# Kernel optimization log

Measured on AMD Instinct MI355X. Metric: run time of the kernel, lower is better.

Reference implementation:

```python
import jax, jax.numpy as jnp
import numpy as np

D = 1024
H = 16
HD = D // H
T = 2048  # tgt_len
S = 2048  # src_len
B = 2


def setup_inputs() -> dict:
    key = jax.random.key(0)
    ks = jax.random.split(key, 8)
    w_scale = (6.0 / (D + D)) ** 0.5  # xavier_uniform bound scale (use normal*small for simplicity)
    inp = {
        "query": jax.random.normal(ks[0], (T, B, D), jnp.float32),
        "key": jax.random.normal(ks[1], (S, B, D), jnp.float32),
        "value": jax.random.normal(ks[2], (S, B, D), jnp.float32),
        "Wq": jax.random.normal(ks[3], (D, D), jnp.float32) * w_scale,
        "bq": jnp.zeros((D,), jnp.float32),
        "Wk": jax.random.normal(ks[4], (D, D), jnp.float32) * w_scale,
        "bk": jnp.zeros((D,), jnp.float32),
        "Wv": jax.random.normal(ks[5], (D, D), jnp.float32) * w_scale,
        "bv": jnp.zeros((D,), jnp.float32),
        "Wo": jax.random.normal(ks[6], (D, D), jnp.float32) * w_scale,
        "bo": jnp.zeros((D,), jnp.float32),
    }
    return inp


def reference(query, key, value, Wq, bq, Wk, bk, Wv, bv, Wo, bo):
    tgt_len, bsz, d = query.shape
    src_len = key.shape[0]
    num_heads, head_dim = H, HD
    scaling = head_dim ** -0.5

    # torch Linear: x @ W.T + b
    q = query @ Wq.T + bq   # [T, B, D]
    k = key @ Wk.T + bk     # [S, B, D]
    v = value @ Wv.T + bv   # [S, B, D]

    q = (q * scaling).reshape(tgt_len, bsz, num_heads, head_dim)
    k = k.reshape(src_len, bsz, num_heads, head_dim)
    v = v.reshape(src_len, bsz, num_heads, head_dim)

    # scores: [B, H, T, S]
    scores = jnp.einsum("tbhd,sbhd->bhts", q, k)
    attn = jax.nn.softmax(scores, axis=-1)
    # dropout_p = 0.0 -> no-op

    # attention output: [T, B, H, HD] -> [T, B, D]
    out = jnp.einsum("bhts,sbhd->tbhd", attn, v).reshape(tgt_len, bsz, d)
    Z = out @ Wo.T + bo  # [T, B, D]

    attn_avg = attn.sum(axis=1) / num_heads  # [B, T, S]
    return Z, attn_avg
```

## Files before the change

### kernel.cpp

```cpp
#include <hip/hip_runtime.h>
#include <hip/hip_bf16.h>
#include <math.h>

#define DD    1024
#define NHEAD 16
#define HDIM  64
#define TLEN  2048
#define SLEN  2048
#define BSZ   2
#define NBH   (BSZ*NHEAD)
#define GROWS (TLEN*BSZ)

typedef _Float16 half8 __attribute__((ext_vector_type(8)));
typedef _Float16 half4v __attribute__((ext_vector_type(4)));
typedef float f32x4 __attribute__((ext_vector_type(4)));

#define MFMA16(a,b,c) __builtin_amdgcn_mfma_f32_16x16x32_f16((a),(b),(c),0,0,0)

#define GLD16(g, l) __builtin_amdgcn_global_load_lds( \
    (const __attribute__((address_space(1))) unsigned int*)(g), \
    (__attribute__((address_space(3))) unsigned int*)(l), 16, 0, 0)

__device__ __forceinline__ int swz(int row, int col2) { return col2 ^ ((row & 7) << 4); }

__global__ __launch_bounds__(256) void convk(const float* __restrict__ s,
                                             _Float16* __restrict__ d, int n8) {
    int i = blockIdx.x * 256 + threadIdx.x;
    if (i >= n8) return;
    const float4* s4 = (const float4*)s;
    float4 a = s4[2*i], b = s4[2*i+1];
    half8 v;
    v[0]=(_Float16)a.x; v[1]=(_Float16)a.y; v[2]=(_Float16)a.z; v[3]=(_Float16)a.w;
    v[4]=(_Float16)b.x; v[5]=(_Float16)b.y; v[6]=(_Float16)b.z; v[7]=(_Float16)b.w;
    *(half8*)&d[8*i] = v;
}

__global__ __launch_bounds__(256) void gemm16(const _Float16* __restrict__ A,
        const _Float16* __restrict__ Bw, const float* __restrict__ bias,
        void* __restrict__ Yp, float scale, int f32out) {
    __shared__ _Float16 As[128*32];
    __shared__ _Float16 Bs[128*32];
    const int tid = threadIdx.x;
    const int lane = tid & 63, w = tid >> 6;
    const int l15 = lane & 15, g = lane >> 4;
    const int m0 = blockIdx.y * 128, n0 = blockIdx.x * 128;
    const int wm = (w >> 1) * 64, wn = (w & 1) * 64;

    f32x4 acc[4][4];
    #pragma unroll
    for (int i = 0; i < 4; ++i)
        #pragma unroll
        for (int j = 0; j < 4; ++j) acc[i][j] = (f32x4){0.f,0.f,0.f,0.f};

    for (int kt = 0; kt < DD/32; ++kt) {
        #pragma unroll
        for (int it = 0; it < 2; ++it) {
            int X = (it*256 + tid) * 16;
            int row = X >> 6, xin = X & 63;
            GLD16(A  + (size_t)(m0+row)*DD + kt*32 + (xin>>1), (char*)As + X);
            GLD16(Bw + (size_t)(n0+row)*DD + kt*32 + (xin>>1), (char*)Bs + X);
        }
        __syncthreads();
        half8 af[4], bf[4];
        #pragma unroll
        for (int i = 0; i < 4; ++i)
            af[i] = *(const half8*)((const char*)As + (wm+16*i+l15)*64 + 16*g);
        #pragma unroll
        for (int j = 0; j < 4; ++j)
            bf[j] = *(const half8*)((const char*)Bs + (wn+16*j+l15)*64 + 16*g);
        #pragma unroll
        for (int i = 0; i < 4; ++i)
            #pragma unroll
            for (int j = 0; j < 4; ++j)
                acc[i][j] = MFMA16(af[i], bf[j], acc[i][j]);
        __syncthreads();
    }

    #pragma unroll
    for (int j = 0; j < 4; ++j) {
        int c = n0 + wn + 16*j + l15;
        float bj = bias[c];
        #pragma unroll
        for (int i = 0; i < 4; ++i) {
            #pragma unroll
            for (int r = 0; r < 4; ++r) {
                int rr = m0 + wm + 16*i + 4*g + r;
                float y = (acc[i][j][r] + bj) * scale;
                if (f32out) ((float*)Yp)[(size_t)rr*DD + c] = y;
                else        ((_Float16*)Yp)[(size_t)rr*DD + c] = (_Float16)y;
            }
        }
    }
}

__global__ __launch_bounds__(256) void transv(const _Float16* __restrict__ Vp,
                                              _Float16* __restrict__ Vt) {
    __shared__ _Float16 Ts[64*64];
    const int tid = threadIdx.x;
    const int s0 = blockIdx.x * 64, bh = blockIdx.y;
    const int b = bh >> 4, h = bh & 15;
    #pragma unroll
    for (int it = 0; it < 2; ++it) {
        int X = (it*256 + tid) * 16;
        int row = X >> 7, xin = X & 127;
        int col2 = swz(row, xin);
        GLD16(Vp + (size_t)((s0+row)*2 + b)*DD + h*64 + (col2>>1), (char*)Ts + X);
    }
    __syncthreads();
    const int d = tid >> 2, sp = tid & 3;
    unsigned int wb[8];
    #pragma unroll
    for (int k = 0; k < 16; ++k) {
        int s = sp*16 + k;
        unsigned short u = *(const unsigned short*)((const char*)Ts + s*128 + swz(s, d*2));
        if (k & 1) wb[k>>1] |= ((unsigned int)u) << 16;
        else       wb[k>>1] = u;
    }
    unsigned int* op = (unsigned int*)(Vt + ((size_t)bh*64 + d)*SLEN + s0 + sp*16);
    ((uint4*)op)[0] = make_uint4(wb[0],wb[1],wb[2],wb[3]);
    ((uint4*)op)[1] = make_uint4(wb[4],wb[5],wb[6],wb[7]);
}

__global__ __launch_bounds__(256) void att_o(const _Float16* __restrict__ Qp,
        const _Float16* __restrict__ Kp, const _Float16* __restrict__ Vt,
        _Float16* __restrict__ Op, float* __restrict__ Ml, float* __restrict__ Il) {
    __shared__ char smem[32768];
    _Float16* Ks  = (_Float16*)smem;
    _Float16* Vts = (_Float16*)(smem + 8192);
    const int tid = threadIdx.x;
    const int lane = tid & 63, w = tid >> 6;
    const int l15 = lane & 15, g = lane >> 4;
    const int bh = blockIdx.y, b = bh >> 4, h = bh & 15;
    const int t0 = blockIdx.x * 128;

    half8 qf[2][2];
    #pragma unroll
    for (int nf = 0; nf < 2; ++nf) {
        int t = t0 + w*32 + 16*nf + l15;
        #pragma unroll
        for (int kq = 0; kq < 2; ++kq)
            qf[nf][kq] = *(const half8*)(Qp + (size_t)(t*2+b)*DD + h*64 + 8*g + 32*kq);
    }

    float m[2] = {-1e30f, -1e30f}, l[2] = {0.f, 0.f};
    f32x4 O[4][2];
    #pragma unroll
    for (int dm = 0; dm < 4; ++dm)
        #pragma unroll
        for (int nf = 0; nf < 2; ++nf) O[dm][nf] = (f32x4){0.f,0.f,0.f,0.f};

    for (int s0 = 0; s0 < SLEN; s0 += 64) {
        #pragma unroll
        for (int it = 0; it < 2; ++it) {
            int X = (it*256 + tid) * 16;
            int row = X >> 7, xin = X & 127;
            int col2 = swz(row, xin);
            GLD16(Kp + (size_t)((s0+row)*2 + b)*DD + h*64 + (col2>>1), (char*)Ks + X);
            GLD16(Vt + ((size_t)bh*64 + row)*SLEN + s0 + (col2>>1), (char*)Vts + X);
        }
        __syncthreads();

        f32x4 sc[4][2];
        #pragma unroll
        for (int mf = 0; mf < 4; ++mf) {
            int srow = 16*mf + l15, sw = (srow & 7) << 4;
            half8 k0 = *(const half8*)((const char*)Ks + srow*128 + ((16*g) ^ sw));
            half8 k1 = *(const half8*)((const char*)Ks + srow*128 + ((64 + 16*g) ^ sw));
            #pragma unroll
            for (int nf = 0; nf < 2; ++nf) {
                f32x4 z = (f32x4){0.f,0.f,0.f,0.f};
                z = MFMA16(k0, qf[nf][0], z);
                z = MFMA16(k1, qf[nf][1], z);
                sc[mf][nf] = z;
            }
        }

        half8 pbf[2][2];
        #pragma unroll
        for (int nf = 0; nf < 2; ++nf) {
            float mx = -1e30f;
            #pragma unroll
            for (int mf = 0; mf < 4; ++mf)
                #pragma unroll
                for (int r = 0; r < 4; ++r) mx = fmaxf(mx, sc[mf][nf][r]);
            mx = fmaxf(mx, __shfl_xor(mx, 16));
            mx = fmaxf(mx, __shfl_xor(mx, 32));
            float mn = fmaxf(m[nf], mx);
            float corr = __expf(m[nf] - mn);
            float pr[4][4];
            float rs = 0.f;
            #pragma unroll
            for (int mf = 0; mf < 4; ++mf)
                #pragma unroll
                for (int r = 0; r < 4; ++r) {
                    pr[mf][r] = __expf(sc[mf][nf][r] - mn);
                    rs += pr[mf][r];
                }
            rs += __shfl_xor(rs, 16);
            rs += __shfl_xor(rs, 32);
            l[nf] = l[nf] * corr + rs;
            m[nf] = mn;
            #pragma unroll
            for (int dm = 0; dm < 4; ++dm) O[dm][nf] *= corr;
            #pragma unroll
            for (int kv = 0; kv < 2; ++kv) {
                half8 pb;
                #pragma unroll
                for (int e = 0; e < 4; ++e) {
                    pb[e]   = (_Float16)pr[2*kv][e];
                    pb[4+e] = (_Float16)pr[2*kv+1][e];
                }
                pbf[nf][kv] = pb;
            }
        }

        #pragma unroll
        for (int dm = 0; dm < 4; ++dm) {
            int dl = 16*dm + l15, sw = (dl & 7) << 4;
            #pragma unroll
            for (int kv = 0; kv < 2; ++kv) {
                half4v a0 = *(const half4v*)((const char*)Vts + dl*128 + ((64*kv + 8*g) ^ sw));
                half4v a1 = *(const half4v*)((const char*)Vts + dl*128 + ((64*kv + 32 + 8*g) ^ sw));
                half8 va;
                #pragma unroll
                for (int e = 0; e < 4; ++e) { va[e] = a0[e]; va[4+e] = a1[e]; }
                #pragma unroll
                for (int nf = 0; nf < 2; ++nf)
                    O[dm][nf] = MFMA16(va, pbf[nf][kv], O[dm][nf]);
            }
        }
        __syncthreads();
    }

    float inv[2];
    #pragma unroll
    for (int nf = 0; nf < 2; ++nf) {
        inv[nf] = 1.f / l[nf];
        #pragma unroll
        for (int dm = 0; dm < 4; ++dm) O[dm][nf] *= inv[nf];
    }
    if (g == 0) {
        #pragma unroll
        for (int nf = 0; nf < 2; ++nf) {
            int t = t0 + w*32 + 16*nf + l15;
            Ml[(size_t)bh*TLEN + t] = m[nf];
            Il[(size_t)bh*TLEN + t] = inv[nf];
        }
    }

    float* ow = (float*)smem;
    #pragma unroll
    for (int nf = 0; nf < 2; ++nf) {
        int tl = w*32 + 16*nf + l15;
        #pragma unroll
        for (int dm = 0; dm < 4; ++dm)
            *(f32x4*)&ow[tl*64 + 16*dm + 4*g] = O[dm][nf];
    }
    __syncthreads();
    {
        int trow = tid >> 1, half = tid & 1;
        const float4* rp = (const float4*)(ow + trow*64 + half*32);
        _Float16* gp = Op + (size_t)((t0+trow)*2 + b)*DD + h*64 + half*32;
        #pragma unroll
        for (int c = 0; c < 4; ++c) {
            float4 x = rp[2*c], y = rp[2*c+1];
            half8 o;
            o[0]=(_Float16)x.x; o[1]=(_Float16)x.y; o[2]=(_Float16)x.z; o[3]=(_Float16)x.w;
            o[4]=(_Float16)y.x; o[5]=(_Float16)y.y; o[6]=(_Float16)y.z; o[7]=(_Float16)y.w;
            ((half8*)gp)[c] = o;
        }
    }
}

__global__ __launch_bounds__(256) void att_avg(const _Float16* __restrict__ Qp,
        const _Float16* __restrict__ Kp, const float* __restrict__ Ml,
        const float* __restrict__ Il, float* __restrict__ avg) {
    __shared__ char smem[32768];
    _Float16* Ks = (_Float16*)smem;
    const int tid = threadIdx.x;
    const int lane = tid & 63, w = tid >> 6;
    const int l15 = lane & 15, g = lane >> 4;
    const int b = blockIdx.z;
    const int t0 = blockIdx.y * 128, s0 = blockIdx.x * 128;

    float acc[8][2][4];
    #pragma unroll
    for (int mf = 0; mf < 8; ++mf)
        #pragma unroll
        for (int nf = 0; nf < 2; ++nf)
            #pragma unroll
            for (int r = 0; r < 4; ++r) acc[mf][nf][r] = 0.f;

    for (int h = 0; h < NHEAD; ++h) {
        const int bh = b*NHEAD + h;
        #pragma unroll
        for (int it = 0; it < 4; ++it) {
            int X = (it*256 + tid) * 16;
            int row = X >> 7, xin = X & 127;
            int col2 = swz(row, xin);
            GLD16(Kp + (size_t)((s0+row)*2 + b)*DD + h*64 + (col2>>1), (char*)Ks + X);
        }
        __syncthreads();

        half8 qf[2][2];
        float mm[2], ii[2];
        #pragma unroll
        for (int nf = 0; nf < 2; ++nf) {
            int t = t0 + w*32 + 16*nf + l15;
            #pragma unroll
            for (int kq = 0; kq < 2; ++kq)
                qf[nf][kq] = *(const half8*)(Qp + (size_t)(t*2+b)*DD + h*64 + 8*g + 32*kq);
            mm[nf] = Ml[(size_t)bh*TLEN + t];
            ii[nf] = Il[(size_t)bh*TLEN + t];
        }

        #pragma unroll
        for (int mf = 0; mf < 8; ++mf) {
            int srow = 16*mf + l15, sw = (srow & 7) << 4;
            half8 k0 = *(const half8*)((const char*)Ks + srow*128 + ((16*g) ^ sw));
            half8 k1 = *(const half8*)((const char*)Ks + srow*128 + ((64 + 16*g) ^ sw));
            #pragma unroll
            for (int nf = 0; nf < 2; ++nf) {
                f32x4 z = (f32x4){0.f,0.f,0.f,0.f};
                z = MFMA16(k0, qf[nf][0], z);
                z = MFMA16(k1, qf[nf][1], z);
                #pragma unroll
                for (int r = 0; r < 4; ++r)
                    acc[mf][nf][r] += __expf(z[r] - mm[nf]) * ii[nf];
            }
        }
        __syncthreads();
    }

    const float invh = 1.f / NHEAD;
    float* ow = (float*)smem;
    #pragma unroll
    for (int P = 0; P < 2; ++P) {
        __syncthreads();
        #pragma unroll
        for (int nf = 0; nf < 2; ++nf) {
            int tl = 16*nf + l15;
            #pragma unroll
            for (int mf2 = 0; mf2 < 4; ++mf2) {
                int mf = 4*P + mf2;
                f32x4 v;
                #pragma unroll
                for (int r = 0; r < 4; ++r) v[r] = acc[mf][nf][r] * invh;
                *(f32x4*)&ow[w*2048 + tl*64 + 16*mf2 + 4*g] = v;
            }
        }
        __syncthreads();
        int trow = tid >> 1, half = tid & 1;
        const float4* rp = (const float4*)(ow + (trow>>5)*2048 + (trow&31)*64 + half*32);
        float4* gp = (float4*)(avg + ((size_t)(b*TLEN + t0 + trow))*SLEN + s0 + P*64 + half*32);
        #pragma unroll
        for (int c = 0; c < 8; ++c) gp[c] = rp[c];
    }
}

extern "C" void kernel_launch(void* const* d_in, const int* in_sizes, int n_in,
                              void* d_out, int out_size, void* d_ws, size_t ws_size,
                              hipStream_t stream) {
    (void)in_sizes; (void)n_in; (void)out_size; (void)ws_size;
    const float* query = (const float*)d_in[0];
    const float* key_  = (const float*)d_in[1];
    const float* value = (const float*)d_in[2];
    const float* Wq = (const float*)d_in[3];  const float* bq = (const float*)d_in[4];
    const float* Wk = (const float*)d_in[5];  const float* bk = (const float*)d_in[6];
    const float* Wv = (const float*)d_in[7];  const float* bv = (const float*)d_in[8];
    const float* Wo = (const float*)d_in[9];  const float* bo = (const float*)d_in[10];

    float* out = (float*)d_out;
    char* ws = (char*)d_ws;
    _Float16* QF  = (_Float16*)(ws);
    _Float16* KF  = (_Float16*)(ws + 8388608);
    _Float16* VF  = (_Float16*)(ws + 16777216);
    _Float16* WqF = (_Float16*)(ws + 25165824);
    _Float16* WkF = (_Float16*)(ws + 27262976);
    _Float16* WvF = (_Float16*)(ws + 29360128);
    _Float16* WoF = (_Float16*)(ws + 31457280);
    _Float16* Qp  = (_Float16*)(ws + 33554432);
    _Float16* Kp  = (_Float16*)(ws + 41943040);
    _Float16* Vp  = (_Float16*)(ws + 50331648);
    _Float16* Vt  = (_Float16*)(ws + 58720256);
    float*    Ml  = (float*)(ws + 67108864);
    float*    Il  = (float*)(ws + 67371008);
    _Float16* Op  = QF;

    const dim3 blk(256);
    convk<<<2048, blk, 0, stream>>>(query, QF, 524288);
    convk<<<2048, blk, 0, stream>>>(key_,  KF, 524288);
    convk<<<2048, blk, 0, stream>>>(value, VF, 524288);
    convk<<<512,  blk, 0, stream>>>(Wq, WqF, 131072);
    convk<<<512,  blk, 0, stream>>>(Wk, WkF, 131072);
    convk<<<512,  blk, 0, stream>>>(Wv, WvF, 131072);
    convk<<<512,  blk, 0, stream>>>(Wo, WoF, 131072);

    const dim3 ggrid(8, 32);
    gemm16<<<ggrid, blk, 0, stream>>>(QF, WqF, bq, Qp, 0.125f, 0);
    gemm16<<<ggrid, blk, 0, stream>>>(KF, WkF, bk, Kp, 1.0f,   0);
    gemm16<<<ggrid, blk, 0, stream>>>(VF, WvF, bv, Vp, 1.0f,   0);

    transv<<<dim3(32, 32), blk, 0, stream>>>(Vp, Vt);
    att_o<<<dim3(16, 32), blk, 0, stream>>>(Qp, Kp, Vt, Op, Ml, Il);
    att_avg<<<dim3(16, 16, 2), blk, 0, stream>>>(Qp, Kp, Ml, Il, out + 4194304);

    gemm16<<<ggrid, blk, 0, stream>>>(Op, WoF, bo, out, 1.0f, 1);
}
```

Baseline: 361.7 us.

## Batch conversions and QKV GEMMs, halve attention tiles, deepen GEMM K-step

```diff
diff --git a/kernel.cpp b/kernel.cpp
--- a/kernel.cpp
+++ b/kernel.cpp
@@ -12,7 +12,6 @@
 #define GROWS (TLEN*BSZ)
 
 typedef _Float16 half8 __attribute__((ext_vector_type(8)));
-typedef _Float16 half4v __attribute__((ext_vector_type(4)));
 typedef float f32x4 __attribute__((ext_vector_type(4)));
 
 #define MFMA16(a,b,c) __builtin_amdgcn_mfma_f32_16x16x32_f16((a),(b),(c),0,0,0)
@@ -23,27 +22,28 @@
 
 __device__ __forceinline__ int swz(int row, int col2) { return col2 ^ ((row & 7) << 4); }
 
-__global__ __launch_bounds__(256) void convk(const float* __restrict__ s,
-                                             _Float16* __restrict__ d, int n8) {
-    int i = blockIdx.x * 256 + threadIdx.x;
-    if (i >= n8) return;
-    const float4* s4 = (const float4*)s;
-    float4 a = s4[2*i], b = s4[2*i+1];
+struct CvtArgs { const float* s[7]; _Float16* d[7]; };
+
+__global__ __launch_bounds__(256) void convall(CvtArgs a) {
+    int idx = blockIdx.x * 256 + threadIdx.x;
+    int ai, wi;
+    if (idx < 1572864) { ai = idx / 524288; wi = idx - ai * 524288; }
+    else { int r = idx - 1572864; ai = 3 + (r >> 17); wi = r & 131071; }
+    const float4* s4 = (const float4*)a.s[ai];
+    float4 x = s4[2*wi], y = s4[2*wi+1];
     half8 v;
-    v[0]=(_Float16)a.x; v[1]=(_Float16)a.y; v[2]=(_Float16)a.z; v[3]=(_Float16)a.w;
-    v[4]=(_Float16)b.x; v[5]=(_Float16)b.y; v[6]=(_Float16)b.z; v[7]=(_Float16)b.w;
-    *(half8*)&d[8*i] = v;
-}
-
-__global__ __launch_bounds__(256) void gemm16(const _Float16* __restrict__ A,
-        const _Float16* __restrict__ Bw, const float* __restrict__ bias,
-        void* __restrict__ Yp, float scale, int f32out) {
-    __shared__ _Float16 As[128*32];
-    __shared__ _Float16 Bs[128*32];
+    v[0]=(_Float16)x.x; v[1]=(_Float16)x.y; v[2]=(_Float16)x.z; v[3]=(_Float16)x.w;
+    v[4]=(_Float16)y.x; v[5]=(_Float16)y.y; v[6]=(_Float16)y.z; v[7]=(_Float16)y.w;
+    *(half8*)&a.d[ai][8*wi] = v;
+}
+
+__device__ __forceinline__ void gemm_body(_Float16* As, _Float16* Bs,
+        const _Float16* __restrict__ A, const _Float16* __restrict__ Bw,
+        const float* __restrict__ bias, void* __restrict__ Yp,
+        float scale, int f32out, int m0, int n0) {
     const int tid = threadIdx.x;
     const int lane = tid & 63, w = tid >> 6;
     const int l15 = lane & 15, g = lane >> 4;
-    const int m0 = blockIdx.y * 128, n0 = blockIdx.x * 128;
     const int wm = (w >> 1) * 64, wn = (w & 1) * 64;
 
     f32x4 acc[4][4];
@@ -52,27 +52,30 @@
         #pragma unroll
         for (int j = 0; j < 4; ++j) acc[i][j] = (f32x4){0.f,0.f,0.f,0.f};
 
-    for (int kt = 0; kt < DD/32; ++kt) {
-        #pragma unroll
-        for (int it = 0; it < 2; ++it) {
+    for (int kt = 0; kt < DD/64; ++kt) {
+        #pragma unroll
+        for (int it = 0; it < 4; ++it) {
             int X = (it*256 + tid) * 16;
-            int row = X >> 6, xin = X & 63;
-            GLD16(A  + (size_t)(m0+row)*DD + kt*32 + (xin>>1), (char*)As + X);
-            GLD16(Bw + (size_t)(n0+row)*DD + kt*32 + (xin>>1), (char*)Bs + X);
-        }
-        __syncthreads();
-        half8 af[4], bf[4];
-        #pragma unroll
-        for (int i = 0; i < 4; ++i)
-            af[i] = *(const half8*)((const char*)As + (wm+16*i+l15)*64 + 16*g);
-        #pragma unroll
-        for (int j = 0; j < 4; ++j)
-            bf[j] = *(const half8*)((const char*)Bs + (wn+16*j+l15)*64 + 16*g);
-        #pragma unroll
-        for (int i = 0; i < 4; ++i)
+            int row = X >> 7, xin = X & 127;
+            GLD16(A  + (size_t)(m0+row)*DD + kt*64 + (xin>>1), (char*)As + X);
+            GLD16(Bw + (size_t)(n0+row)*DD + kt*64 + (xin>>1), (char*)Bs + X);
+        }
+        __syncthreads();
+        #pragma unroll
+        for (int kq = 0; kq < 2; ++kq) {
+            half8 af[4], bf[4];
+            #pragma unroll
+            for (int i = 0; i < 4; ++i)
+                af[i] = *(const half8*)((const char*)As + (wm+16*i+l15)*128 + 16*g + 64*kq);
             #pragma unroll
             for (int j = 0; j < 4; ++j)
-                acc[i][j] = MFMA16(af[i], bf[j], acc[i][j]);
+                bf[j] = *(const half8*)((const char*)Bs + (wn+16*j+l15)*128 + 16*g + 64*kq);
+            #pragma unroll
+            for (int i = 0; i < 4; ++i)
+                #pragma unroll
+                for (int j = 0; j < 4; ++j)
+                    acc[i][j] = MFMA16(af[i], bf[j], acc[i][j]);
+        }
         __syncthreads();
     }
 
@@ -93,6 +96,30 @@
     }
 }
 
+__global__ __launch_bounds__(256) void gemm_qkv(
+        const _Float16* QF, const _Float16* KF, const _Float16* VF,
+        const _Float16* WqF, const _Float16* WkF, const _Float16* WvF,
+        const float* bq, const float* bk, const float* bv,
+        _Float16* Qp, _Float16* Kp, _Float16* Vp) {
+    __shared__ _Float16 As[128*64];
+    __shared__ _Float16 Bs[128*64];
+    const int z = blockIdx.z;
+    const _Float16* A  = (z == 0) ? QF  : (z == 1) ? KF  : VF;
+    const _Float16* Wm = (z == 0) ? WqF : (z == 1) ? WkF : WvF;
+    const float*    bi = (z == 0) ? bq  : (z == 1) ? bk  : bv;
+    _Float16*       Y  = (z == 0) ? Qp  : (z == 1) ? Kp  : Vp;
+    float scale = (z == 0) ? 0.125f : 1.0f;
+    gemm_body(As, Bs, A, Wm, bi, Y, scale, 0, blockIdx.y*128, blockIdx.x*128);
+}
+
+__global__ __launch_bounds__(256) void gemm_out(const _Float16* __restrict__ A,
+        const _Float16* __restrict__ Wm, const float* __restrict__ bi,
+        float* __restrict__ Y) {
+    __shared__ _Float16 As[128*64];
+    __shared__ _Float16 Bs[128*64];
+    gemm_body(As, Bs, A, Wm, bi, Y, 1.0f, 1, blockIdx.y*128, blockIdx.x*128);
+}
+
 __global__ __launch_bounds__(256) void transv(const _Float16* __restrict__ Vp,
                                               _Float16* __restrict__ Vt) {
     __shared__ _Float16 Ts[64*64];
@@ -108,46 +135,43 @@
     }
     __syncthreads();
     const int d = tid >> 2, sp = tid & 3;
-    unsigned int wb[8];
-    #pragma unroll
-    for (int k = 0; k < 16; ++k) {
-        int s = sp*16 + k;
-        unsigned short u = *(const unsigned short*)((const char*)Ts + s*128 + swz(s, d*2));
-        if (k & 1) wb[k>>1] |= ((unsigned int)u) << 16;
-        else       wb[k>>1] = u;
-    }
-    unsigned int* op = (unsigned int*)(Vt + ((size_t)bh*64 + d)*SLEN + s0 + sp*16);
-    ((uint4*)op)[0] = make_uint4(wb[0],wb[1],wb[2],wb[3]);
-    ((uint4*)op)[1] = make_uint4(wb[4],wb[5],wb[6],wb[7]);
+    _Float16* rowp = Vt + ((size_t)bh*64 + d)*SLEN + s0 + 32*(sp>>1) + 4*(sp&1);
+    #pragma unroll
+    for (int j = 0; j < 4; ++j) {
+        unsigned short us[4];
+        #pragma unroll
+        for (int e = 0; e < 4; ++e) {
+            int s = 16*sp + 4*j + e;
+            us[e] = *(const unsigned short*)((const char*)Ts + s*128 + swz(s, d*2));
+        }
+        uint2 pk = make_uint2(us[0] | ((unsigned)us[1] << 16),
+                              us[2] | ((unsigned)us[3] << 16));
+        *(uint2*)(rowp + 8*j) = pk;
+    }
 }
 
 __global__ __launch_bounds__(256) void att_o(const _Float16* __restrict__ Qp,
         const _Float16* __restrict__ Kp, const _Float16* __restrict__ Vt,
         _Float16* __restrict__ Op, float* __restrict__ Ml, float* __restrict__ Il) {
-    __shared__ char smem[32768];
+    __shared__ char smem[16384];
     _Float16* Ks  = (_Float16*)smem;
     _Float16* Vts = (_Float16*)(smem + 8192);
     const int tid = threadIdx.x;
     const int lane = tid & 63, w = tid >> 6;
     const int l15 = lane & 15, g = lane >> 4;
     const int bh = blockIdx.y, b = bh >> 4, h = bh & 15;
-    const int t0 = blockIdx.x * 128;
-
-    half8 qf[2][2];
-    #pragma unroll
-    for (int nf = 0; nf < 2; ++nf) {
-        int t = t0 + w*32 + 16*nf + l15;
-        #pragma unroll
-        for (int kq = 0; kq < 2; ++kq)
-            qf[nf][kq] = *(const half8*)(Qp + (size_t)(t*2+b)*DD + h*64 + 8*g + 32*kq);
-    }
-
-    float m[2] = {-1e30f, -1e30f}, l[2] = {0.f, 0.f};
-    f32x4 O[4][2];
-    #pragma unroll
-    for (int dm = 0; dm < 4; ++dm)
-        #pragma unroll
-        for (int nf = 0; nf < 2; ++nf) O[dm][nf] = (f32x4){0.f,0.f,0.f,0.f};
+    const int t0 = blockIdx.x * 64;
+    const int t = t0 + w*16 + l15;
+
+    half8 qf[2];
+    #pragma unroll
+    for (int kq = 0; kq < 2; ++kq)
+        qf[kq] = *(const half8*)(Qp + (size_t)(t*2+b)*DD + h*64 + 8*g + 32*kq);
+
+    float m = -1e30f, l = 0.f;
+    f32x4 O[4];
+    #pragma unroll
+    for (int dm = 0; dm < 4; ++dm) O[dm] = (f32x4){0.f,0.f,0.f,0.f};
 
     for (int s0 = 0; s0 < SLEN; s0 += 64) {
         #pragma unroll
@@ -160,58 +184,53 @@
         }
         __syncthreads();
 
-        f32x4 sc[4][2];
+        f32x4 sc[4];
         #pragma unroll
         for (int mf = 0; mf < 4; ++mf) {
             int srow = 16*mf + l15, sw = (srow & 7) << 4;
             half8 k0 = *(const half8*)((const char*)Ks + srow*128 + ((16*g) ^ sw));
             half8 k1 = *(const half8*)((const char*)Ks + srow*128 + ((64 + 16*g) ^ sw));
-            #pragma unroll
-            for (int nf = 0; nf < 2; ++nf) {
-                f32x4 z = (f32x4){0.f,0.f,0.f,0.f};
-                z = MFMA16(k0, qf[nf][0], z);
-                z = MFMA16(k1, qf[nf][1], z);
-                sc[mf][nf] = z;
+            f32x4 z = (f32x4){0.f,0.f,0.f,0.f};
+            z = MFMA16(k0, qf[0], z);
+            z = MFMA16(k1, qf[1], z);
+            sc[mf] = z;
+        }
+
+        float mx = -1e30f;
+        #pragma unroll
+        for (int mf = 0; mf < 4; ++mf)
+            #pragma unroll
+            for (int r = 0; r < 4; ++r) mx = fmaxf(mx, sc[mf][r]);
+        mx = fmaxf(mx, __shfl_xor(mx, 16));
+        mx = fmaxf(mx, __shfl_xor(mx, 32));
+        float mn = fmaxf(m, mx);
+        float corr = __expf(m - mn);
+        float pr[4][4];
+        float rs = 0.f;
+        #pragma unroll
+        for (int mf = 0; mf < 4; ++mf)
+            #pragma unroll
+            for (int r = 0; r < 4; ++r) {
+                pr[mf][r] = __expf(sc[mf][r] - mn);
+                rs += pr[mf][r];
             }
-        }
-
-        half8 pbf[2][2];
-        #pragma unroll
-        for (int nf = 0; nf < 2; ++nf) {
-            float mx = -1e30f;
-            #pragma unroll
-            for (int mf = 0; mf < 4; ++mf)
-                #pragma unroll
-                for (int r = 0; r < 4; ++r) mx = fmaxf(mx, sc[mf][nf][r]);
-            mx = fmaxf(mx, __shfl_xor(mx, 16));
-            mx = fmaxf(mx, __shfl_xor(mx, 32));
-            float mn = fmaxf(m[nf], mx);
-            float corr = __expf(m[nf] - mn);
-            float pr[4][4];
-            float rs = 0.f;
-            #pragma unroll
-            for (int mf = 0; mf < 4; ++mf)
-                #pragma unroll
-                for (int r = 0; r < 4; ++r) {
-                    pr[mf][r] = __expf(sc[mf][nf][r] - mn);
-                    rs += pr[mf][r];
-                }
-            rs += __shfl_xor(rs, 16);
-            rs += __shfl_xor(rs, 32);
-            l[nf] = l[nf] * corr + rs;
-            m[nf] = mn;
-            #pragma unroll
-            for (int dm = 0; dm < 4; ++dm) O[dm][nf] *= corr;
-            #pragma unroll
-            for (int kv = 0; kv < 2; ++kv) {
-                half8 pb;
-                #pragma unroll
-                for (int e = 0; e < 4; ++e) {
-                    pb[e]   = (_Float16)pr[2*kv][e];
-                    pb[4+e] = (_Float16)pr[2*kv+1][e];
-                }
-                pbf[nf][kv] = pb;
+        rs += __shfl_xor(rs, 16);
+        rs += __shfl_xor(rs, 32);
+        l = l * corr + rs;
+        m = mn;
+        #pragma unroll
+        for (int dm = 0; dm < 4; ++dm) O[dm] *= corr;
+
+        half8 pbf[2];
+        #pragma unroll
+        for (int kv = 0; kv < 2; ++kv) {
+            half8 pb;
+            #pragma unroll
+            for (int e = 0; e < 4; ++e) {
+                pb[e]   = (_Float16)pr[2*kv][e];
+                pb[4+e] = (_Float16)pr[2*kv+1][e];
             }
+            pbf[kv] = pb;
         }
 
         #pragma unroll
@@ -219,50 +238,35 @@
             int dl = 16*dm + l15, sw = (dl & 7) << 4;
             #pragma unroll
             for (int kv = 0; kv < 2; ++kv) {
-                half4v a0 = *(const half4v*)((const char*)Vts + dl*128 + ((64*kv + 8*g) ^ sw));
-                half4v a1 = *(const half4v*)((const char*)Vts + dl*128 + ((64*kv + 32 + 8*g) ^ sw));
-                half8 va;
-                #pragma unroll
-                for (int e = 0; e < 4; ++e) { va[e] = a0[e]; va[4+e] = a1[e]; }
-                #pragma unroll
-                for (int nf = 0; nf < 2; ++nf)
-                    O[dm][nf] = MFMA16(va, pbf[nf][kv], O[dm][nf]);
+                half8 va = *(const half8*)((const char*)Vts + dl*128 + ((64*kv + 16*g) ^ sw));
+                O[dm] = MFMA16(va, pbf[kv], O[dm]);
             }
         }
         __syncthreads();
     }
 
-    float inv[2];
-    #pragma unroll
-    for (int nf = 0; nf < 2; ++nf) {
-        inv[nf] = 1.f / l[nf];
-        #pragma unroll
-        for (int dm = 0; dm < 4; ++dm) O[dm][nf] *= inv[nf];
-    }
+    float inv = 1.f / l;
+    #pragma unroll
+    for (int dm = 0; dm < 4; ++dm) O[dm] *= inv;
     if (g == 0) {
-        #pragma unroll
-        for (int nf = 0; nf < 2; ++nf) {
-            int t = t0 + w*32 + 16*nf + l15;
-            Ml[(size_t)bh*TLEN + t] = m[nf];
-            Il[(size_t)bh*TLEN + t] = inv[nf];
-        }
+        Ml[(size_t)bh*TLEN + t] = m;
+        Il[(size_t)bh*TLEN + t] = inv;
     }
 
     float* ow = (float*)smem;
-    #pragma unroll
-    for (int nf = 0; nf < 2; ++nf) {
-        int tl = w*32 + 16*nf + l15;
+    {
+        int tl = w*16 + l15;
         #pragma unroll
         for (int dm = 0; dm < 4; ++dm)
-            *(f32x4*)&ow[tl*64 + 16*dm + 4*g] = O[dm][nf];
+            *(f32x4*)&ow[tl*64 + 16*dm + 4*g] = O[dm];
     }
     __syncthreads();
     {
-        int trow = tid >> 1, half = tid & 1;
-        const float4* rp = (const float4*)(ow + trow*64 + half*32);
-        _Float16* gp = Op + (size_t)((t0+trow)*2 + b)*DD + h*64 + half*32;
-        #pragma unroll
-        for (int c = 0; c < 4; ++c) {
+        int trow = tid >> 2, q = tid & 3;
+        const float4* rp = (const float4*)(ow + trow*64 + q*16);
+        _Float16* gp = Op + (size_t)((t0+trow)*2 + b)*DD + h*64 + q*16;
+        #pragma unroll
+        for (int c = 0; c < 2; ++c) {
             float4 x = rp[2*c], y = rp[2*c+1];
             half8 o;
             o[0]=(_Float16)x.x; o[1]=(_Float16)x.y; o[2]=(_Float16)x.z; o[3]=(_Float16)x.w;
@@ -281,18 +285,18 @@
     const int lane = tid & 63, w = tid >> 6;
     const int l15 = lane & 15, g = lane >> 4;
     const int b = blockIdx.z;
-    const int t0 = blockIdx.y * 128, s0 = blockIdx.x * 128;
-
-    float acc[8][2][4];
+    const int t0 = blockIdx.y * 64, s0 = blockIdx.x * 128;
+    const int t = t0 + w*16 + l15;
+
+    float acc[8][4];
     #pragma unroll
     for (int mf = 0; mf < 8; ++mf)
         #pragma unroll
-        for (int nf = 0; nf < 2; ++nf)
-            #pragma unroll
-            for (int r = 0; r < 4; ++r) acc[mf][nf][r] = 0.f;
+        for (int r = 0; r < 4; ++r) acc[mf][r] = 0.f;
 
     for (int h = 0; h < NHEAD; ++h) {
         const int bh = b*NHEAD + h;
+        __syncthreads();
         #pragma unroll
         for (int it = 0; it < 4; ++it) {
             int X = (it*256 + tid) * 16;
@@ -302,57 +306,45 @@
         }
         __syncthreads();
 
-        half8 qf[2][2];
-        float mm[2], ii[2];
-        #pragma unroll
-        for (int nf = 0; nf < 2; ++nf) {
-            int t = t0 + w*32 + 16*nf + l15;
-            #pragma unroll
-            for (int kq = 0; kq < 2; ++kq)
-                qf[nf][kq] = *(const half8*)(Qp + (size_t)(t*2+b)*DD + h*64 + 8*g + 32*kq);
-            mm[nf] = Ml[(size_t)bh*TLEN + t];
-            ii[nf] = Il[(size_t)bh*TLEN + t];
-        }
+        half8 qf[2];
+        #pragma unroll
+        for (int kq = 0; kq < 2; ++kq)
+            qf[kq] = *(const half8*)(Qp + (size_t)(t*2+b)*DD + h*64 + 8*g + 32*kq);
+        float mm = Ml[(size_t)bh*TLEN + t];
+        float ii = Il[(size_t)bh*TLEN + t];
 
         #pragma unroll
         for (int mf = 0; mf < 8; ++mf) {
             int srow = 16*mf + l15, sw = (srow & 7) << 4;
             half8 k0 = *(const half8*)((const char*)Ks + srow*128 + ((16*g) ^ sw));
             half8 k1 = *(const half8*)((const char*)Ks + srow*128 + ((64 + 16*g) ^ sw));
-            #pragma unroll
-            for (int nf = 0; nf < 2; ++nf) {
-                f32x4 z = (f32x4){0.f,0.f,0.f,0.f};
-                z = MFMA16(k0, qf[nf][0], z);
-                z = MFMA16(k1, qf[nf][1], z);
-                #pragma unroll
-                for (int r = 0; r < 4; ++r)
-                    acc[mf][nf][r] += __expf(z[r] - mm[nf]) * ii[nf];
-            }
-        }
-        __syncthreads();
-    }
-
+            f32x4 z = (f32x4){0.f,0.f,0.f,0.f};
+            z = MFMA16(k0, qf[0], z);
+            z = MFMA16(k1, qf[1], z);
+            #pragma unroll
+            for (int r = 0; r < 4; ++r)
+                acc[mf][r] += __expf(z[r] - mm) * ii;
+        }
+    }
+
+    __syncthreads();
     const float invh = 1.f / NHEAD;
     float* ow = (float*)smem;
-    #pragma unroll
-    for (int P = 0; P < 2; ++P) {
-        __syncthreads();
-        #pragma unroll
-        for (int nf = 0; nf < 2; ++nf) {
-            int tl = 16*nf + l15;
-            #pragma unroll
-            for (int mf2 = 0; mf2 < 4; ++mf2) {
-                int mf = 4*P + mf2;
-                f32x4 v;
-                #pragma unroll
-                for (int r = 0; r < 4; ++r) v[r] = acc[mf][nf][r] * invh;
-                *(f32x4*)&ow[w*2048 + tl*64 + 16*mf2 + 4*g] = v;
-            }
-        }
-        __syncthreads();
-        int trow = tid >> 1, half = tid & 1;
-        const float4* rp = (const float4*)(ow + (trow>>5)*2048 + (trow&31)*64 + half*32);
-        float4* gp = (float4*)(avg + ((size_t)(b*TLEN + t0 + trow))*SLEN + s0 + P*64 + half*32);
+    {
+        int tl = w*16 + l15;
+        #pragma unroll
+        for (int mf = 0; mf < 8; ++mf) {
+            f32x4 v;
+            #pragma unroll
+            for (int r = 0; r < 4; ++r) v[r] = acc[mf][r] * invh;
+            *(f32x4*)&ow[tl*128 + 16*mf + 4*g] = v;
+        }
+    }
+    __syncthreads();
+    {
+        int trow = tid >> 2, q = tid & 3;
+        const float4* rp = (const float4*)(ow + trow*128 + q*32);
+        float4* gp = (float4*)(avg + ((size_t)(b*TLEN + t0 + trow))*SLEN + s0 + q*32);
         #pragma unroll
         for (int c = 0; c < 8; ++c) gp[c] = rp[c];
     }
@@ -388,22 +380,18 @@
     _Float16* Op  = QF;
 
     const dim3 blk(256);
-    convk<<<2048, blk, 0, stream>>>(query, QF, 524288);
-    convk<<<2048, blk, 0, stream>>>(key_,  KF, 524288);
-    convk<<<2048, blk, 0, stream>>>(value, VF, 524288);
-    convk<<<512,  blk, 0, stream>>>(Wq, WqF, 131072);
-    convk<<<512,  blk, 0, stream>>>(Wk, WkF, 131072);
-    convk<<<512,  blk, 0, stream>>>(Wv, WvF, 131072);
-    convk<<<512,  blk, 0, stream>>>(Wo, WoF, 131072);
-
-    const dim3 ggrid(8, 32);
-    gemm16<<<ggrid, blk, 0, stream>>>(QF, WqF, bq, Qp, 0.125f, 0);
-    gemm16<<<ggrid, blk, 0, stream>>>(KF, WkF, bk, Kp, 1.0f,   0);
-    gemm16<<<ggrid, blk, 0, stream>>>(VF, WvF, bv, Vp, 1.0f,   0);
+
+    CvtArgs ca;
+    ca.s[0]=query; ca.s[1]=key_; ca.s[2]=value; ca.s[3]=Wq; ca.s[4]=Wk; ca.s[5]=Wv; ca.s[6]=Wo;
+    ca.d[0]=QF;    ca.d[1]=KF;   ca.d[2]=VF;    ca.d[3]=WqF; ca.d[4]=WkF; ca.d[5]=WvF; ca.d[6]=WoF;
+    convall<<<8192, blk, 0, stream>>>(ca);
+
+    gemm_qkv<<<dim3(8, 32, 3), blk, 0, stream>>>(QF, KF, VF, WqF, WkF, WvF,
+                                                 bq, bk, bv, Qp, Kp, Vp);
 
     transv<<<dim3(32, 32), blk, 0, stream>>>(Vp, Vt);
-    att_o<<<dim3(16, 32), blk, 0, stream>>>(Qp, Kp, Vt, Op, Ml, Il);
-    att_avg<<<dim3(16, 16, 2), blk, 0, stream>>>(Qp, Kp, Ml, Il, out + 4194304);
-
-    gemm16<<<ggrid, blk, 0, stream>>>(Op, WoF, bo, out, 1.0f, 1);
-}
+    att_o<<<dim3(32, 32), blk, 0, stream>>>(Qp, Kp, Vt, Op, Ml, Il);
+    att_avg<<<dim3(16, 32, 2), blk, 0, stream>>>(Qp, Kp, Ml, Il, out + 4194304);
+
+    gemm_out<<<dim3(8, 32), blk, 0, stream>>>(Op, WoF, bo, out);
+}
```

New measurement: 321.4 us. 11.1% less time.
